# Kernel tuning notes

Measured on AMD Instinct MI355X. Metric: run time of the kernel, lower is better.

## Reference

```python
import jax, jax.numpy as jnp
import numpy as np

S, B, H = 2048, 32, 1024


def setup_inputs() -> dict:
    key = jax.random.key(0)
    k1, k2, k3, k4 = jax.random.split(key, 4)
    hidden = jax.random.normal(k1, (B, H), dtype=jnp.float32)
    encoder_outputs = jax.random.normal(k2, (S, B, H), dtype=jnp.float32)
    # nn.Linear(H, H): weight [H, H] (applied as x @ W^T), bias [H]
    W = jax.random.normal(k3, (H, H), dtype=jnp.float32) / np.sqrt(H)
    b = jax.random.normal(k4, (H,), dtype=jnp.float32) / np.sqrt(H)
    return {"hidden": hidden, "encoder_outputs": encoder_outputs, "W": W, "b": b}


def reference(hidden, encoder_outputs, W, b):
    # energy[s,b,:] = Linear(encoder_outputs[s,b,:]) = enc @ W^T + b
    energy = jnp.einsum('sbh,kh->sbk', encoder_outputs, W) + b  # [S,B,H]
    # score[b,s] = hidden[b] . energy[s,b]  (the diag-of-matmul in the loop)
    attn_energies = jnp.einsum('bh,sbh->bs', hidden, energy)  # [B,S]
    after_softmax = jax.nn.softmax(attn_energies, axis=1)      # softmax over seq_len
    return after_softmax[None, :, :]  # [1,B,S]
```

## Files before the change

### kernel.cpp

```cpp
#include <hip/hip_runtime.h>

#define SEQ 2048
#define BATCH 32
#define HID 1024
#define SPW 8

__global__ void __launch_bounds__(256) vproj_kernel(const float* __restrict__ hidden,
                                                    const float* __restrict__ W,
                                                    float* __restrict__ v) {
    const int b  = blockIdx.x;
    const int hc = blockIdx.y;
    const int t  = threadIdx.x;
    const int h4 = hc * 32 + (t & 31);
    const int kk = t >> 5;

    __shared__ float  sh[HID];
    __shared__ float4 red[256];

    ((float4*)sh)[t] = ((const float4*)(hidden + b * HID))[t];
    __syncthreads();

    const float4* __restrict__ W4 = (const float4*)W;
    float4 acc = make_float4(0.f, 0.f, 0.f, 0.f);
    const int k0 = kk * 128;
#pragma unroll 8
    for (int k = k0; k < k0 + 128; ++k) {
        const float  hk = sh[k];
        const float4 w  = W4[k * (HID / 4) + h4];
        acc.x = fmaf(hk, w.x, acc.x);
        acc.y = fmaf(hk, w.y, acc.y);
        acc.z = fmaf(hk, w.z, acc.z);
        acc.w = fmaf(hk, w.w, acc.w);
    }

    red[t] = acc;
    __syncthreads();
    if (t < 128) {
        float4 a = red[t], c = red[t + 128];
        a.x += c.x; a.y += c.y; a.z += c.z; a.w += c.w;
        red[t] = a;
    }
    __syncthreads();
    if (t < 64) {
        float4 a = red[t], c = red[t + 64];
        a.x += c.x; a.y += c.y; a.z += c.z; a.w += c.w;
        red[t] = a;
    }
    __syncthreads();
    if (t < 32) {
        float4 a = red[t], c = red[t + 32];
        a.x += c.x; a.y += c.y; a.z += c.z; a.w += c.w;
        ((float4*)v)[b * (HID / 4) + hc * 32 + t] = a;
    }
}

__global__ void __launch_bounds__(256, 8) score_kernel(const float* __restrict__ enc,
                                                       const float* __restrict__ v,
                                                       float* __restrict__ scores) {
    const int sx   = blockIdx.x;
    const int wave = threadIdx.x >> 6;
    const int lane = threadIdx.x & 63;
    const int b    = blockIdx.y * 4 + wave;

    const float4* __restrict__ v4 = (const float4*)(v + b * HID);
    const float4 w0 = v4[0 * 64 + lane];
    const float4 w1 = v4[1 * 64 + lane];
    const float4 w2 = v4[2 * 64 + lane];
    const float4 w3 = v4[3 * 64 + lane];

    const int s0 = sx * SPW;
#pragma unroll 1
    for (int i = 0; i < SPW; ++i) {
        const int s = s0 + i;
        const float4* __restrict__ e4 =
            (const float4*)(enc + ((size_t)s * BATCH + b) * HID);
        const float4 e0 = e4[0 * 64 + lane];
        const float4 e1 = e4[1 * 64 + lane];
        const float4 e2 = e4[2 * 64 + lane];
        const float4 e3 = e4[3 * 64 + lane];

        float acc = 0.f;
        acc = fmaf(e0.x, w0.x, acc); acc = fmaf(e0.y, w0.y, acc);
        acc = fmaf(e0.z, w0.z, acc); acc = fmaf(e0.w, w0.w, acc);
        acc = fmaf(e1.x, w1.x, acc); acc = fmaf(e1.y, w1.y, acc);
        acc = fmaf(e1.z, w1.z, acc); acc = fmaf(e1.w, w1.w, acc);
        acc = fmaf(e2.x, w2.x, acc); acc = fmaf(e2.y, w2.y, acc);
        acc = fmaf(e2.z, w2.z, acc); acc = fmaf(e2.w, w2.w, acc);
        acc = fmaf(e3.x, w3.x, acc); acc = fmaf(e3.y, w3.y, acc);
        acc = fmaf(e3.z, w3.z, acc); acc = fmaf(e3.w, w3.w, acc);

#pragma unroll
        for (int off = 32; off > 0; off >>= 1) acc += __shfl_xor(acc, off, 64);
        if (lane == 0) scores[b * SEQ + s] = acc;
    }
}

__global__ void __launch_bounds__(256) softmax_kernel(const float* __restrict__ scores,
                                                      float* __restrict__ out) {
    const int b = blockIdx.x;
    const int t = threadIdx.x;
    __shared__ float red[256];

    float x[8];
    float m = -INFINITY;
#pragma unroll
    for (int j = 0; j < 8; ++j) {
        x[j] = scores[b * SEQ + t + j * 256];
        m = fmaxf(m, x[j]);
    }
    red[t] = m;
    __syncthreads();
    for (int o = 128; o > 0; o >>= 1) {
        if (t < o) red[t] = fmaxf(red[t], red[t + o]);
        __syncthreads();
    }
    m = red[0];
    __syncthreads();

    float sum = 0.f;
#pragma unroll
    for (int j = 0; j < 8; ++j) {
        x[j] = __expf(x[j] - m);
        sum += x[j];
    }
    red[t] = sum;
    __syncthreads();
    for (int o = 128; o > 0; o >>= 1) {
        if (t < o) red[t] += red[t + o];
        __syncthreads();
    }
    const float inv = 1.f / red[0];
#pragma unroll
    for (int j = 0; j < 8; ++j) out[b * SEQ + t + j * 256] = x[j] * inv;
}

extern "C" void kernel_launch(void* const* d_in, const int* in_sizes, int n_in,
                              void* d_out, int out_size, void* d_ws, size_t ws_size,
                              hipStream_t stream) {
    const float* hidden = (const float*)d_in[0];
    const float* enc    = (const float*)d_in[1];
    const float* W      = (const float*)d_in[2];
    float* out = (float*)d_out;

    float* v      = (float*)d_ws;
    float* scores = out;

    vproj_kernel<<<dim3(BATCH, 8), 256, 0, stream>>>(hidden, W, v);
    score_kernel<<<dim3(SEQ / SPW, BATCH / 4), 256, 0, stream>>>(enc, v, scores);
    softmax_kernel<<<BATCH, 256, 0, stream>>>(scores, out);
}
```

Measured before the change: 379.8 us.

## Fuse softmax into score kernel via last-block atomic counter

Removes the separate softmax launch. Each score block increments a per-batch-group counter, and the last block to finish for a group runs the softmax, one wave per batch row, using wave shuffles instead of shared-memory reductions. This saves a kernel launch and its tail, at the cost of an atomic and fence in every block, a serialized softmax done by only 8 blocks, and lower occupancy from launch bounds of 4 and a larger register array.

```diff
diff --git a/kernel.cpp b/kernel.cpp
--- a/kernel.cpp
+++ b/kernel.cpp
@@ -7,12 +7,15 @@
 
 __global__ void __launch_bounds__(256) vproj_kernel(const float* __restrict__ hidden,
                                                     const float* __restrict__ W,
-                                                    float* __restrict__ v) {
+                                                    float* __restrict__ v,
+                                                    unsigned* __restrict__ counters) {
     const int b  = blockIdx.x;
     const int hc = blockIdx.y;
     const int t  = threadIdx.x;
     const int h4 = hc * 32 + (t & 31);
     const int kk = t >> 5;
+
+    if (b == 0 && hc == 0 && t < 8) counters[t] = 0u;
 
     __shared__ float  sh[HID];
     __shared__ float4 red[256];
@@ -54,9 +57,9 @@
     }
 }
 
-__global__ void __launch_bounds__(256, 8) score_kernel(const float* __restrict__ enc,
-                                                       const float* __restrict__ v,
-                                                       float* __restrict__ scores) {
+__global__ void __launch_bounds__(256, 4) score_softmax_kernel(
+        const float* __restrict__ enc, const float* __restrict__ v,
+        float* __restrict__ scores, unsigned* __restrict__ counters) {
     const int sx   = blockIdx.x;
     const int wave = threadIdx.x >> 6;
     const int lane = threadIdx.x & 63;
@@ -93,45 +96,37 @@
         for (int off = 32; off > 0; off >>= 1) acc += __shfl_xor(acc, off, 64);
         if (lane == 0) scores[b * SEQ + s] = acc;
     }
-}
 
-__global__ void __launch_bounds__(256) softmax_kernel(const float* __restrict__ scores,
-                                                      float* __restrict__ out) {
-    const int b = blockIdx.x;
-    const int t = threadIdx.x;
-    __shared__ float red[256];
+    __syncthreads();
+    __threadfence();
+    __shared__ unsigned last;
+    if (threadIdx.x == 0) last = atomicAdd(&counters[blockIdx.y], 1u);
+    __syncthreads();
+    if (last != (SEQ / SPW) - 1) return;
+    __threadfence();
+    if (threadIdx.x == 0) counters[blockIdx.y] = 0u;
 
-    float x[8];
+    float x[32];
     float m = -INFINITY;
 #pragma unroll
-    for (int j = 0; j < 8; ++j) {
-        x[j] = scores[b * SEQ + t + j * 256];
+    for (int j = 0; j < 32; ++j) {
+        x[j] = scores[b * SEQ + j * 64 + lane];
         m = fmaxf(m, x[j]);
     }
-    red[t] = m;
-    __syncthreads();
-    for (int o = 128; o > 0; o >>= 1) {
-        if (t < o) red[t] = fmaxf(red[t], red[t + o]);
-        __syncthreads();
-    }
-    m = red[0];
-    __syncthreads();
+#pragma unroll
+    for (int off = 32; off > 0; off >>= 1) m = fmaxf(m, __shfl_xor(m, off, 64));
 
     float sum = 0.f;
 #pragma unroll
-    for (int j = 0; j < 8; ++j) {
+    for (int j = 0; j < 32; ++j) {
         x[j] = __expf(x[j] - m);
         sum += x[j];
     }
-    red[t] = sum;
-    __syncthreads();
-    for (int o = 128; o > 0; o >>= 1) {
-        if (t < o) red[t] += red[t + o];
-        __syncthreads();
-    }
-    const float inv = 1.f / red[0];
 #pragma unroll
-    for (int j = 0; j < 8; ++j) out[b * SEQ + t + j * 256] = x[j] * inv;
+    for (int off = 32; off > 0; off >>= 1) sum += __shfl_xor(sum, off, 64);
+    const float inv = 1.f / sum;
+#pragma unroll
+    for (int j = 0; j < 32; ++j) scores[b * SEQ + j * 64 + lane] = x[j] * inv;
 }
 
 extern "C" void kernel_launch(void* const* d_in, const int* in_sizes, int n_in,
@@ -142,10 +137,11 @@
     const float* W      = (const float*)d_in[2];
     float* out = (float*)d_out;
 
-    float* v      = (float*)d_ws;
-    float* scores = out;
+    float* v           = (float*)d_ws;
+    unsigned* counters = (unsigned*)(v + BATCH * HID);
+    float* scores      = out;
 
-    vproj_kernel<<<dim3(BATCH, 8), 256, 0, stream>>>(hidden, W, v);
-    score_kernel<<<dim3(SEQ / SPW, BATCH / 4), 256, 0, stream>>>(enc, v, scores);
-    softmax_kernel<<<BATCH, 256, 0, stream>>>(scores, out);
+    vproj_kernel<<<dim3(BATCH, 8), 256, 0, stream>>>(hidden, W, v, counters);
+    score_softmax_kernel<<<dim3(SEQ / SPW, BATCH / 4), 256, 0, stream>>>(
+        enc, v, scores, counters);
 }
```

After: 734.3 us. 1.93x slower.
